# Optimization experiments

Measured on AMD Instinct MI355X. Metric: run time of the kernel, lower is better.

Reference implementation:

```python
import jax, jax.numpy as jnp
import numpy as np

B, S, D, KC = 32, 4096, 64, 256  # batch*heads, seq_len, head_dim, compressed dim


def setup_inputs() -> dict:
    key = jax.random.key(0)
    ks = jax.random.split(key, 7)
    return {
        "Q": jax.random.normal(ks[0], (B, S, D), dtype=jnp.float32),
        "K": jax.random.normal(ks[1], (B, S, D), dtype=jnp.float32),
        "V": jax.random.normal(ks[2], (B, S, D), dtype=jnp.float32),
        "E_w": jax.random.normal(ks[3], (KC, S), dtype=jnp.float32) * (1.0 / np.sqrt(S)),
        "E_b": jax.random.normal(ks[4], (KC,), dtype=jnp.float32) * 0.01,
        "F_w": jax.random.normal(ks[5], (KC, S), dtype=jnp.float32) * (1.0 / np.sqrt(S)),
        "F_b": jax.random.normal(ks[6], (KC,), dtype=jnp.float32) * 0.01,
    }


def reference(Q, K, V, E_w, E_b, F_w, F_b):
    # K: [B,S,D] -> transpose -> [B,D,S]; E proj over seq axis -> [B,D,KC]
    Ke = jnp.einsum("bsd,ks->bdk", K, E_w) + E_b  # [B, D, KC]
    # scores: Q @ E(K) -> [B, S, KC], scaled by sqrt(head_dim)
    scale = jnp.sqrt(jnp.asarray(D, dtype=Q.dtype))
    P = jnp.einsum("bsd,bdk->bsk", Q, Ke) / scale
    # causal mask: torch.triu(ones(S, KC)) keeps (i, j) where j >= i
    i = jnp.arange(S)[:, None]
    j = jnp.arange(KC)[None, :]
    keep = j >= i  # [S, KC]
    P = jnp.where(keep[None, :, :], P, jnp.asarray(-1e10, dtype=P.dtype))
    P = jax.nn.softmax(P, axis=-1)  # dropout p=0.0 -> identity
    # V: [B,S,D] -> [B,D,S]; F proj -> [B,D,KC]; transpose -> [B,KC,D]
    Vf = jnp.einsum("bsd,ks->bkd", V, F_w) + F_b[None, :, None]  # [B, KC, D]
    out = jnp.einsum("bsk,bkd->bsd", P, Vf)  # [B, S, D]
    return out
```

## Files before the change

kernel.cpp:

```cpp
#include <hip/hip_runtime.h>
#include <hip/hip_bf16.h>
#include <math.h>

#define NB  32
#define NS  4096
#define ND  64
#define NKC 256

#define BK   128
#define KHALF 2048
#define ASA  132
#define ASB  132

#define QSTR  72
#define PBSTR 264
#define VSTR  264

typedef __attribute__((ext_vector_type(8))) short short8;
typedef __attribute__((ext_vector_type(4))) float f32x4;

__device__ __forceinline__ short f2bf(float f) {
    union { float f; unsigned u; } v; v.f = f;
    return (short)((v.u + 0x7FFFu + ((v.u >> 16) & 1u)) >> 16);
}

__global__ __launch_bounds__(256) void prep(
    const float* __restrict__ Ew, const float* __restrict__ Fw,
    short* __restrict__ EwB, short* __restrict__ FwB)
{
    const int gid = blockIdx.x * 256 + threadIdx.x;
    const int half = (NKC * NS) / 8;
    const float* src = (gid < half) ? Ew : Fw;
    short* dst       = (gid < half) ? EwB : FwB;
    const int i8 = (gid < half) ? gid : gid - half;
    float4 a = *(const float4*)&src[(size_t)i8 * 8];
    float4 c = *(const float4*)&src[(size_t)i8 * 8 + 4];
    short8 w;
    w[0] = f2bf(a.x); w[1] = f2bf(a.y); w[2] = f2bf(a.z); w[3] = f2bf(a.w);
    w[4] = f2bf(c.x); w[5] = f2bf(c.y); w[6] = f2bf(c.z); w[7] = f2bf(c.w);
    *(short8*)&dst[(size_t)i8 * 8] = w;
}

template <typename AT>
__global__ __launch_bounds__(256, 2) void proj_sk(
    const AT* __restrict__ EwX, const AT* __restrict__ FwX,
    const float* __restrict__ K, const float* __restrict__ V,
    float* __restrict__ KeTa, float* __restrict__ Vfa,
    float* __restrict__ KeTb, float* __restrict__ Vfb)
{
    const int bid = blockIdx.x;
    const int r8 = bid & 7, mt = (bid >> 3) & 3, gq = bid >> 5;
    const int grp = gq * 8 + r8;
    const int kh = grp & 1, mm = (grp >> 1) & 1, b = grp >> 2;

    const AT* __restrict__ Ab    = mm ? FwX : EwX;
    const float* __restrict__ Bg = mm ? V   : K;
    float* __restrict__ Cout = kh ? (mm ? Vfb : KeTb) : (mm ? Vfa : KeTa);

    const int t = threadIdx.x, wave = t >> 6, lane = t & 63;
    const int lm = lane & 15, g4 = lane >> 4;
    __shared__ short As[64 * ASA];
    __shared__ short Bs[64 * ASB];
    const size_t bBase = (size_t)b * NS * ND;
    const size_t aBase = (size_t)mt * 64 * NS;
    const int rA = t >> 4, jA = t & 15;
    const int dB = t & 31, sB = t >> 5;

    f32x4 acc[4];
#pragma unroll
    for (int nt = 0; nt < 4; ++nt) acc[nt] = (f32x4){0.f, 0.f, 0.f, 0.f};

    short8 pa[4];
    float4 paf[8];
    float2 pb[16];

    const int sBeg = kh * KHALF, sEnd = sBeg + KHALF;

#pragma unroll
    for (int i = 0; i < 4; ++i) {
        if constexpr (sizeof(AT) == 2) {
            pa[i] = *(const short8*)&Ab[aBase + (size_t)(i * 16 + rA) * NS + sBeg + jA * 8];
        } else {
            paf[2 * i]     = *(const float4*)&Ab[aBase + (size_t)(i * 16 + rA) * NS + sBeg + jA * 8];
            paf[2 * i + 1] = *(const float4*)&Ab[aBase + (size_t)(i * 16 + rA) * NS + sBeg + jA * 8 + 4];
        }
    }
#pragma unroll
    for (int h = 0; h < 2; ++h)
#pragma unroll
        for (int i = 0; i < 8; ++i)
            pb[h * 8 + i] = *(const float2*)&Bg[bBase + (size_t)(sBeg + h * 64 + sB * 8 + i) * ND + dB * 2];

    for (int s0 = sBeg; s0 < sEnd; s0 += BK) {
#pragma unroll
        for (int i = 0; i < 4; ++i) {
            if constexpr (sizeof(AT) == 2) {
                *(short8*)&As[(i * 16 + rA) * ASA + jA * 8] = pa[i];
            } else {
                short8 w;
                w[0] = f2bf(paf[2 * i].x);     w[1] = f2bf(paf[2 * i].y);
                w[2] = f2bf(paf[2 * i].z);     w[3] = f2bf(paf[2 * i].w);
                w[4] = f2bf(paf[2 * i + 1].x); w[5] = f2bf(paf[2 * i + 1].y);
                w[6] = f2bf(paf[2 * i + 1].z); w[7] = f2bf(paf[2 * i + 1].w);
                *(short8*)&As[(i * 16 + rA) * ASA + jA * 8] = w;
            }
        }
#pragma unroll
        for (int h = 0; h < 2; ++h) {
            short8 w0, w1;
#pragma unroll
            for (int i = 0; i < 8; ++i) {
                w0[i] = f2bf(pb[h * 8 + i].x);
                w1[i] = f2bf(pb[h * 8 + i].y);
            }
            *(short8*)&Bs[(dB * 2 + 0) * ASB + h * 64 + sB * 8] = w0;
            *(short8*)&Bs[(dB * 2 + 1) * ASB + h * 64 + sB * 8] = w1;
        }
        __syncthreads();

        if (s0 + BK < sEnd) {
            const int sn = s0 + BK;
#pragma unroll
            for (int i = 0; i < 4; ++i) {
                if constexpr (sizeof(AT) == 2) {
                    pa[i] = *(const short8*)&Ab[aBase + (size_t)(i * 16 + rA) * NS + sn + jA * 8];
                } else {
                    paf[2 * i]     = *(const float4*)&Ab[aBase + (size_t)(i * 16 + rA) * NS + sn + jA * 8];
                    paf[2 * i + 1] = *(const float4*)&Ab[aBase + (size_t)(i * 16 + rA) * NS + sn + jA * 8 + 4];
                }
            }
#pragma unroll
            for (int h = 0; h < 2; ++h)
#pragma unroll
                for (int i = 0; i < 8; ++i)
                    pb[h * 8 + i] = *(const float2*)&Bg[bBase + (size_t)(sn + h * 64 + sB * 8 + i) * ND + dB * 2];
        }

#pragma unroll
        for (int ks = 0; ks < BK; ks += 32) {
            short8 aF = *(const short8*)&As[(wave * 16 + lm) * ASA + ks + g4 * 8];
#pragma unroll
            for (int nt = 0; nt < 4; ++nt) {
                short8 bF = *(const short8*)&Bs[(nt * 16 + lm) * ASB + ks + g4 * 8];
                acc[nt] = __builtin_amdgcn_mfma_f32_16x16x32_bf16(aF, bF, acc[nt], 0, 0, 0);
            }
        }
        __syncthreads();
    }

#pragma unroll
    for (int nt = 0; nt < 4; ++nt)
#pragma unroll
        for (int rr = 0; rr < 4; ++rr) {
            int kc = mt * 64 + wave * 16 + g4 * 4 + rr;
            Cout[((size_t)b * NKC + kc) * ND + nt * 16 + lm] = acc[nt][rr];
        }
}

__global__ __launch_bounds__(256) void reduce2(
    float4* __restrict__ Areg, const float4* __restrict__ Breg)
{
    const int gid = blockIdx.x * 256 + threadIdx.x;
    float4 a = Areg[gid], c = Breg[gid];
    Areg[gid] = (float4){a.x + c.x, a.y + c.y, a.z + c.z, a.w + c.w};
}

__global__ __launch_bounds__(256) void attn_fused(
    const float* __restrict__ Q,  const float* __restrict__ KeT,
    const float* __restrict__ Vf, const float* __restrict__ Eb,
    const float* __restrict__ Fb, float* __restrict__ out)
{
    const int x = blockIdx.x, b = blockIdx.y, t = threadIdx.x;

    if (x >= 8) {
        __shared__ float pq[16][64];
        __shared__ float mv[64];
        const int kg = t >> 4, dq = t & 15;
        float4 s4 = (float4){0.f, 0.f, 0.f, 0.f};
        for (int p = 0; p < 16; ++p) {
            int k = p * 16 + kg;
            float4 v = *(const float4*)&Vf[((size_t)b * NKC + k) * ND + dq * 4];
            float fb = Fb[k];
            s4.x += v.x + fb; s4.y += v.y + fb; s4.z += v.z + fb; s4.w += v.w + fb;
        }
        *(float4*)&pq[kg][dq * 4] = s4;
        __syncthreads();
        if (t < 64) {
            float m = 0.f;
#pragma unroll
            for (int i = 0; i < 16; ++i) m += pq[i][t];
            mv[t] = m * (1.f / 256.f);
        }
        __syncthreads();
        const int r0 = 256 + (x - 8) * 64;
#pragma unroll
        for (int i = 0; i < 4; ++i) {
            int idx = i * 256 + t, row = idx >> 4, q = idx & 15;
            *(float4*)&out[((size_t)b * NS + r0 + row) * ND + q * 4] =
                *(const float4*)&mv[q * 4];
        }
        return;
    }

    const int s0 = x * 32;
    const int wave = t >> 6, lane = t & 63, lm = lane & 15, g = lane >> 4;
    __shared__ short Qs[32 * QSTR];
    __shared__ short PsB[32 * PBSTR];
    __shared__ short VfT[64 * VSTR];
    __shared__ float rsums[32][4];

    {
        int row = t >> 3, dq = t & 7;
        size_t off = ((size_t)b * NS + s0 + row) * ND + dq * 8;
        float4 q0 = *(const float4*)&Q[off], q1 = *(const float4*)&Q[off + 4];
        short8 w;
        w[0] = f2bf(q0.x); w[1] = f2bf(q0.y); w[2] = f2bf(q0.z); w[3] = f2bf(q0.w);
        w[4] = f2bf(q1.x); w[5] = f2bf(q1.y); w[6] = f2bf(q1.z); w[7] = f2bf(q1.w);
        *(short8*)&Qs[row * QSTR + dq * 8] = w;
    }
    {
        const int dB = t & 31, sB = t >> 5;
#pragma unroll
        for (int pass = 0; pass < 4; ++pass) {
            int kb = pass * 64 + sB * 8;
            float2 v[8]; float fb[8];
#pragma unroll
            for (int i = 0; i < 8; ++i) {
                v[i]  = *(const float2*)&Vf[((size_t)b * NKC + kb + i) * ND + dB * 2];
                fb[i] = Fb[kb + i];
            }
            short8 w0, w1;
#pragma unroll
            for (int i = 0; i < 8; ++i) {
                w0[i] = f2bf(v[i].x + fb[i]);
                w1[i] = f2bf(v[i].y + fb[i]);
            }
            *(short8*)&VfT[(dB * 2 + 0) * VSTR + kb] = w0;
            *(short8*)&VfT[(dB * 2 + 1) * VSTR + kb] = w1;
        }
    }
    __syncthreads();

    f32x4 accP[2][4];
#pragma unroll
    for (int rt = 0; rt < 2; ++rt)
#pragma unroll
        for (int kk = 0; kk < 4; ++kk) accP[rt][kk] = (f32x4){0.f, 0.f, 0.f, 0.f};
#pragma unroll
    for (int kk = 0; kk < 4; ++kk) {
        int kt = wave * 4 + kk;
        float ebv = Eb[kt * 16 + lm];
#pragma unroll
        for (int ks2 = 0; ks2 < 2; ++ks2) {
            const float* kp = &KeT[((size_t)b * NKC + kt * 16 + lm) * ND + ks2 * 32 + g * 8];
            float4 c0 = *(const float4*)kp, c1 = *(const float4*)(kp + 4);
            short8 bf;
            bf[0] = f2bf(c0.x + ebv); bf[1] = f2bf(c0.y + ebv);
            bf[2] = f2bf(c0.z + ebv); bf[3] = f2bf(c0.w + ebv);
            bf[4] = f2bf(c1.x + ebv); bf[5] = f2bf(c1.y + ebv);
            bf[6] = f2bf(c1.z + ebv); bf[7] = f2bf(c1.w + ebv);
#pragma unroll
            for (int rt = 0; rt < 2; ++rt) {
                short8 aq = *(const short8*)&Qs[(rt * 16 + lm) * QSTR + ks2 * 32 + g * 8];
                accP[rt][kk] = __builtin_amdgcn_mfma_f32_16x16x32_bf16(aq, bf, accP[rt][kk], 0, 0, 0);
            }
        }
    }
#pragma unroll
    for (int rt = 0; rt < 2; ++rt)
#pragma unroll
        for (int r = 0; r < 4; ++r) {
            float s = 0.f;
            int rowg = s0 + rt * 16 + g * 4 + r;
#pragma unroll
            for (int kk = 0; kk < 4; ++kk) {
                int col = wave * 64 + kk * 16 + lm;
                float e = (col >= rowg) ? __expf(accP[rt][kk][r] * 0.125f) : 0.f;
                accP[rt][kk][r] = e;
                s += e;
            }
#pragma unroll
            for (int off = 1; off <= 8; off <<= 1) s += __shfl_xor(s, off, 64);
            if (lm == 0) rsums[rt * 16 + g * 4 + r][wave] = s;
        }
    __syncthreads();
#pragma unroll
    for (int rt = 0; rt < 2; ++rt)
#pragma unroll
        for (int r = 0; r < 4; ++r) {
            float4 rs = *(const float4*)&rsums[rt * 16 + g * 4 + r][0];
            float inv = 1.f / (rs.x + rs.y + rs.z + rs.w);
#pragma unroll
            for (int kk = 0; kk < 4; ++kk)
                PsB[(rt * 16 + g * 4 + r) * PBSTR + wave * 64 + kk * 16 + lm] =
                    f2bf(accP[rt][kk][r] * inv);
        }
    __syncthreads();

    f32x4 oa[2];
    oa[0] = (f32x4){0.f, 0.f, 0.f, 0.f};
    oa[1] = (f32x4){0.f, 0.f, 0.f, 0.f};
    for (int ks = x; ks < 8; ++ks) {
        short8 bv = *(const short8*)&VfT[(wave * 16 + lm) * VSTR + ks * 32 + g * 8];
#pragma unroll
        for (int rt = 0; rt < 2; ++rt) {
            short8 av = *(const short8*)&PsB[(rt * 16 + lm) * PBSTR + ks * 32 + g * 8];
            oa[rt] = __builtin_amdgcn_mfma_f32_16x16x32_bf16(av, bv, oa[rt], 0, 0, 0);
        }
    }
#pragma unroll
    for (int rt = 0; rt < 2; ++rt)
#pragma unroll
        for (int r = 0; r < 4; ++r)
            out[((size_t)b * NS + s0 + rt * 16 + g * 4 + r) * ND + wave * 16 + lm] = oa[rt][r];
}

extern "C" void kernel_launch(void* const* d_in, const int* in_sizes, int n_in,
                              void* d_out, int out_size, void* d_ws, size_t ws_size,
                              hipStream_t stream) {
    (void)in_sizes; (void)n_in; (void)out_size;
    const float* Q  = (const float*)d_in[0];
    const float* K  = (const float*)d_in[1];
    const float* V  = (const float*)d_in[2];
    const float* Ew = (const float*)d_in[3];
    const float* Eb = (const float*)d_in[4];
    const float* Fw = (const float*)d_in[5];
    const float* Fb = (const float*)d_in[6];
    float* out = (float*)d_out;

    const size_t nKe = (size_t)NB * NKC * ND;
    float* base = (float*)d_ws;
    float* KeTa = base;
    float* Vfa  = base + nKe;
    float* KeTb = base + 2 * nKe;
    float* Vfb  = base + 3 * nKe;

    if (ws_size >= 12u * 1024 * 1024) {
        short* EwB = (short*)(base + 4 * nKe);
        short* FwB = EwB + (size_t)NKC * NS;
        prep<<<dim3(1024), 256, 0, stream>>>(Ew, Fw, EwB, FwB);
        proj_sk<short><<<dim3(512), 256, 0, stream>>>(EwB, FwB, K, V,
                                                      KeTa, Vfa, KeTb, Vfb);
    } else {
        proj_sk<float><<<dim3(512), 256, 0, stream>>>(Ew, Fw, K, V,
                                                      KeTa, Vfa, KeTb, Vfb);
    }
    reduce2<<<dim3(1024), 256, 0, stream>>>((float4*)base,
                                            (const float4*)(base + 2 * nKe));
    attn_fused<<<dim3(68, NB), 256, 0, stream>>>(Q, KeTa, Vfa, Eb, Fb, out);
}
```

Measured before the change: 185.6 us.

## Drop weight prep, fuse split-K reduce with bias/bf16 conversion before attention

Removes the separate bf16 conversion pass over E_w/F_w, so proj_sk always reads fp32 weights directly. Replaces the reduce2 kernel with a fuse kernel that sums the two split-K halves, adds biases, and writes bf16 Ke and a pre-transposed bf16 Vf plus partial column sums. The attention kernel then loads ready bf16 tiles and reduces the partial sums for the masked-row mean instead of redoing conversion per block. This trades one conversion kernel for heavier fp32 weight traffic in the projection, and the workspace threshold decides which path runs.

```diff
diff --git a/kernel.cpp b/kernel.cpp
--- a/kernel.cpp
+++ b/kernel.cpp
@@ -7,46 +7,30 @@
 #define ND  64
 #define NKC 256
 
-#define BK   128
+#define BK    128
 #define KHALF 2048
-#define ASA  132
-#define ASB  132
+#define ASA   132
+#define ASB   132
 
 #define QSTR  72
 #define PBSTR 264
 #define VSTR  264
 
+#define NKE ((size_t)NB * NKC * ND)
+
 typedef __attribute__((ext_vector_type(8))) short short8;
 typedef __attribute__((ext_vector_type(4))) float f32x4;
 
 __device__ __forceinline__ short f2bf(float f) {
     union { float f; unsigned u; } v; v.f = f;
     return (short)((v.u + 0x7FFFu + ((v.u >> 16) & 1u)) >> 16);
-}
-
-__global__ __launch_bounds__(256) void prep(
-    const float* __restrict__ Ew, const float* __restrict__ Fw,
-    short* __restrict__ EwB, short* __restrict__ FwB)
-{
-    const int gid = blockIdx.x * 256 + threadIdx.x;
-    const int half = (NKC * NS) / 8;
-    const float* src = (gid < half) ? Ew : Fw;
-    short* dst       = (gid < half) ? EwB : FwB;
-    const int i8 = (gid < half) ? gid : gid - half;
-    float4 a = *(const float4*)&src[(size_t)i8 * 8];
-    float4 c = *(const float4*)&src[(size_t)i8 * 8 + 4];
-    short8 w;
-    w[0] = f2bf(a.x); w[1] = f2bf(a.y); w[2] = f2bf(a.z); w[3] = f2bf(a.w);
-    w[4] = f2bf(c.x); w[5] = f2bf(c.y); w[6] = f2bf(c.z); w[7] = f2bf(c.w);
-    *(short8*)&dst[(size_t)i8 * 8] = w;
 }
 
 template <typename AT>
 __global__ __launch_bounds__(256, 2) void proj_sk(
     const AT* __restrict__ EwX, const AT* __restrict__ FwX,
     const float* __restrict__ K, const float* __restrict__ V,
-    float* __restrict__ KeTa, float* __restrict__ Vfa,
-    float* __restrict__ KeTb, float* __restrict__ Vfb)
+    float* __restrict__ base)
 {
     const int bid = blockIdx.x;
     const int r8 = bid & 7, mt = (bid >> 3) & 3, gq = bid >> 5;
@@ -55,7 +39,7 @@
 
     const AT* __restrict__ Ab    = mm ? FwX : EwX;
     const float* __restrict__ Bg = mm ? V   : K;
-    float* __restrict__ Cout = kh ? (mm ? Vfb : KeTb) : (mm ? Vfa : KeTa);
+    float* __restrict__ Cout = base + (size_t)kh * 2 * NKE + (mm ? NKE : 0);
 
     const int t = threadIdx.x, wave = t >> 6, lane = t & 63;
     const int lm = lane & 15, g4 = lane >> 4;
@@ -157,39 +141,56 @@
         }
 }
 
-__global__ __launch_bounds__(256) void reduce2(
-    float4* __restrict__ Areg, const float4* __restrict__ Breg)
-{
-    const int gid = blockIdx.x * 256 + threadIdx.x;
-    float4 a = Areg[gid], c = Breg[gid];
-    Areg[gid] = (float4){a.x + c.x, a.y + c.y, a.z + c.z, a.w + c.w};
-}
-
-__global__ __launch_bounds__(256) void attn_fused(
-    const float* __restrict__ Q,  const float* __restrict__ KeT,
-    const float* __restrict__ Vf, const float* __restrict__ Eb,
-    const float* __restrict__ Fb, float* __restrict__ out)
+__global__ __launch_bounds__(256) void fuse(
+    const float* __restrict__ base, const float* __restrict__ Eb,
+    const float* __restrict__ Fb, short* __restrict__ KeB,
+    short* __restrict__ VtB, float* __restrict__ ps)
 {
     const int x = blockIdx.x, b = blockIdx.y, t = threadIdx.x;
+    const int kb = x * 16;
+    const float* Ka  = base;
+    const float* Va  = base + NKE;
+    const float* Kb_ = base + 2 * NKE;
+    const float* Vb  = base + 3 * NKE;
+    __shared__ float vt[16][65];
+    const int kci = t >> 6, d = t & 63;
+
+#pragma unroll
+    for (int i = 0; i < 4; ++i) {
+        int kc = kb + kci * 4 + i;
+        size_t off = ((size_t)b * NKC + kc) * ND + d;
+        KeB[off] = f2bf(Ka[off] + Kb_[off] + Eb[kc]);
+        vt[kci * 4 + i][d] = Va[off] + Vb[off] + Fb[kc];
+    }
+    __syncthreads();
+    if (t < 64) {
+        float s = 0.f;
+        short8 w0, w1;
+#pragma unroll
+        for (int i = 0; i < 8; ++i) { float v = vt[i][t];     s += v; w0[i] = f2bf(v); }
+#pragma unroll
+        for (int i = 0; i < 8; ++i) { float v = vt[8 + i][t]; s += v; w1[i] = f2bf(v); }
+        ps[((size_t)b * 16 + x) * 64 + t] = s;
+        short* dst = &VtB[((size_t)b * ND + t) * NKC + kb];
+        *(short8*)&dst[0] = w0;
+        *(short8*)&dst[8] = w1;
+    }
+}
+
+__global__ __launch_bounds__(256) void attn_new(
+    const float* __restrict__ Q,  const short* __restrict__ KeB,
+    const short* __restrict__ VtB, const float* __restrict__ ps,
+    float* __restrict__ out)
+{
+    const int x = blockIdx.x, b = blockIdx.y, t = threadIdx.x;
 
     if (x >= 8) {
-        __shared__ float pq[16][64];
-        __shared__ float mv[64];
-        const int kg = t >> 4, dq = t & 15;
-        float4 s4 = (float4){0.f, 0.f, 0.f, 0.f};
-        for (int p = 0; p < 16; ++p) {
-            int k = p * 16 + kg;
-            float4 v = *(const float4*)&Vf[((size_t)b * NKC + k) * ND + dq * 4];
-            float fb = Fb[k];
-            s4.x += v.x + fb; s4.y += v.y + fb; s4.z += v.z + fb; s4.w += v.w + fb;
-        }
-        *(float4*)&pq[kg][dq * 4] = s4;
-        __syncthreads();
+        __shared__ float mvs[64];
         if (t < 64) {
-            float m = 0.f;
-#pragma unroll
-            for (int i = 0; i < 16; ++i) m += pq[i][t];
-            mv[t] = m * (1.f / 256.f);
+            float s = 0.f;
+#pragma unroll
+            for (int i = 0; i < 16; ++i) s += ps[((size_t)b * 16 + i) * 64 + t];
+            mvs[t] = s * (1.f / 256.f);
         }
         __syncthreads();
         const int r0 = 256 + (x - 8) * 64;
@@ -197,7 +198,7 @@
         for (int i = 0; i < 4; ++i) {
             int idx = i * 256 + t, row = idx >> 4, q = idx & 15;
             *(float4*)&out[((size_t)b * NS + r0 + row) * ND + q * 4] =
-                *(const float4*)&mv[q * 4];
+                *(const float4*)&mvs[q * 4];
         }
         return;
     }
@@ -219,6 +220,141 @@
         *(short8*)&Qs[row * QSTR + dq * 8] = w;
     }
     {
+        const int d = t >> 2, q4 = t & 3;
+        const short* src = &VtB[((size_t)b * ND + d) * NKC + q4 * 64];
+#pragma unroll
+        for (int i = 0; i < 8; ++i)
+            *(short8*)&VfT[d * VSTR + q4 * 64 + i * 8] = *(const short8*)&src[i * 8];
+    }
+    __syncthreads();
+
+    f32x4 accP[2][4];
+#pragma unroll
+    for (int rt = 0; rt < 2; ++rt)
+#pragma unroll
+        for (int kk = 0; kk < 4; ++kk) accP[rt][kk] = (f32x4){0.f, 0.f, 0.f, 0.f};
+#pragma unroll
+    for (int kk = 0; kk < 4; ++kk) {
+        int kt = wave * 4 + kk;
+#pragma unroll
+        for (int ks2 = 0; ks2 < 2; ++ks2) {
+            short8 bf = *(const short8*)&KeB[((size_t)b * NKC + kt * 16 + lm) * ND + ks2 * 32 + g * 8];
+#pragma unroll
+            for (int rt = 0; rt < 2; ++rt) {
+                short8 aq = *(const short8*)&Qs[(rt * 16 + lm) * QSTR + ks2 * 32 + g * 8];
+                accP[rt][kk] = __builtin_amdgcn_mfma_f32_16x16x32_bf16(aq, bf, accP[rt][kk], 0, 0, 0);
+            }
+        }
+    }
+#pragma unroll
+    for (int rt = 0; rt < 2; ++rt)
+#pragma unroll
+        for (int r = 0; r < 4; ++r) {
+            float s = 0.f;
+            int rowg = s0 + rt * 16 + g * 4 + r;
+#pragma unroll
+            for (int kk = 0; kk < 4; ++kk) {
+                int col = wave * 64 + kk * 16 + lm;
+                float e = (col >= rowg) ? __expf(accP[rt][kk][r] * 0.125f) : 0.f;
+                accP[rt][kk][r] = e;
+                s += e;
+            }
+#pragma unroll
+            for (int off = 1; off <= 8; off <<= 1) s += __shfl_xor(s, off, 64);
+            if (lm == 0) rsums[rt * 16 + g * 4 + r][wave] = s;
+        }
+    __syncthreads();
+#pragma unroll
+    for (int rt = 0; rt < 2; ++rt)
+#pragma unroll
+        for (int r = 0; r < 4; ++r) {
+            float4 rs = *(const float4*)&rsums[rt * 16 + g * 4 + r][0];
+            float inv = 1.f / (rs.x + rs.y + rs.z + rs.w);
+#pragma unroll
+            for (int kk = 0; kk < 4; ++kk)
+                PsB[(rt * 16 + g * 4 + r) * PBSTR + wave * 64 + kk * 16 + lm] =
+                    f2bf(accP[rt][kk][r] * inv);
+        }
+    __syncthreads();
+
+    f32x4 oa[2];
+    oa[0] = (f32x4){0.f, 0.f, 0.f, 0.f};
+    oa[1] = (f32x4){0.f, 0.f, 0.f, 0.f};
+    for (int ks = x; ks < 8; ++ks) {
+        short8 bv = *(const short8*)&VfT[(wave * 16 + lm) * VSTR + ks * 32 + g * 8];
+#pragma unroll
+        for (int rt = 0; rt < 2; ++rt) {
+            short8 av = *(const short8*)&PsB[(rt * 16 + lm) * PBSTR + ks * 32 + g * 8];
+            oa[rt] = __builtin_amdgcn_mfma_f32_16x16x32_bf16(av, bv, oa[rt], 0, 0, 0);
+        }
+    }
+#pragma unroll
+    for (int rt = 0; rt < 2; ++rt)
+#pragma unroll
+        for (int r = 0; r < 4; ++r)
+            out[((size_t)b * NS + s0 + rt * 16 + g * 4 + r) * ND + wave * 16 + lm] = oa[rt][r];
+}
+
+__global__ __launch_bounds__(256) void attn_old(
+    const float* __restrict__ Q,  const float* __restrict__ base,
+    const float* __restrict__ Eb, const float* __restrict__ Fb,
+    float* __restrict__ out)
+{
+    const int x = blockIdx.x, b = blockIdx.y, t = threadIdx.x;
+    const float* KeTa = base;
+    const float* Vfa  = base + NKE;
+    const float* KeTb = base + 2 * NKE;
+    const float* Vfb  = base + 3 * NKE;
+
+    if (x >= 8) {
+        __shared__ float pq[16][64];
+        __shared__ float mvs[64];
+        const int kg = t >> 4, dq = t & 15;
+        float4 s4 = (float4){0.f, 0.f, 0.f, 0.f};
+        for (int p = 0; p < 16; ++p) {
+            int k = p * 16 + kg;
+            float4 v = *(const float4*)&Vfa[((size_t)b * NKC + k) * ND + dq * 4];
+            float4 u = *(const float4*)&Vfb[((size_t)b * NKC + k) * ND + dq * 4];
+            float fb = Fb[k];
+            s4.x += (v.x + u.x) + fb; s4.y += (v.y + u.y) + fb;
+            s4.z += (v.z + u.z) + fb; s4.w += (v.w + u.w) + fb;
+        }
+        *(float4*)&pq[kg][dq * 4] = s4;
+        __syncthreads();
+        if (t < 64) {
+            float m = 0.f;
+#pragma unroll
+            for (int i = 0; i < 16; ++i) m += pq[i][t];
+            mvs[t] = m * (1.f / 256.f);
+        }
+        __syncthreads();
+        const int r0 = 256 + (x - 8) * 64;
+#pragma unroll
+        for (int i = 0; i < 4; ++i) {
+            int idx = i * 256 + t, row = idx >> 4, q = idx & 15;
+            *(float4*)&out[((size_t)b * NS + r0 + row) * ND + q * 4] =
+                *(const float4*)&mvs[q * 4];
+        }
+        return;
+    }
+
+    const int s0 = x * 32;
+    const int wave = t >> 6, lane = t & 63, lm = lane & 15, g = lane >> 4;
+    __shared__ short Qs[32 * QSTR];
+    __shared__ short PsB[32 * PBSTR];
+    __shared__ short VfT[64 * VSTR];
+    __shared__ float rsums[32][4];
+
+    {
+        int row = t >> 3, dq = t & 7;
+        size_t off = ((size_t)b * NS + s0 + row) * ND + dq * 8;
+        float4 q0 = *(const float4*)&Q[off], q1 = *(const float4*)&Q[off + 4];
+        short8 w;
+        w[0] = f2bf(q0.x); w[1] = f2bf(q0.y); w[2] = f2bf(q0.z); w[3] = f2bf(q0.w);
+        w[4] = f2bf(q1.x); w[5] = f2bf(q1.y); w[6] = f2bf(q1.z); w[7] = f2bf(q1.w);
+        *(short8*)&Qs[row * QSTR + dq * 8] = w;
+    }
+    {
         const int dB = t & 31, sB = t >> 5;
 #pragma unroll
         for (int pass = 0; pass < 4; ++pass) {
@@ -226,7 +362,9 @@
             float2 v[8]; float fb[8];
 #pragma unroll
             for (int i = 0; i < 8; ++i) {
-                v[i]  = *(const float2*)&Vf[((size_t)b * NKC + kb + i) * ND + dB * 2];
+                float2 a = *(const float2*)&Vfa[((size_t)b * NKC + kb + i) * ND + dB * 2];
+                float2 c = *(const float2*)&Vfb[((size_t)b * NKC + kb + i) * ND + dB * 2];
+                v[i]  = (float2){a.x + c.x, a.y + c.y};
                 fb[i] = Fb[kb + i];
             }
             short8 w0, w1;
@@ -252,13 +390,14 @@
         float ebv = Eb[kt * 16 + lm];
 #pragma unroll
         for (int ks2 = 0; ks2 < 2; ++ks2) {
-            const float* kp = &KeT[((size_t)b * NKC + kt * 16 + lm) * ND + ks2 * 32 + g * 8];
-            float4 c0 = *(const float4*)kp, c1 = *(const float4*)(kp + 4);
+            const size_t koff = ((size_t)b * NKC + kt * 16 + lm) * ND + ks2 * 32 + g * 8;
+            float4 c0 = *(const float4*)&KeTa[koff], c1 = *(const float4*)&KeTa[koff + 4];
+            float4 e0 = *(const float4*)&KeTb[koff], e1 = *(const float4*)&KeTb[koff + 4];
             short8 bf;
-            bf[0] = f2bf(c0.x + ebv); bf[1] = f2bf(c0.y + ebv);
-            bf[2] = f2bf(c0.z + ebv); bf[3] = f2bf(c0.w + ebv);
-            bf[4] = f2bf(c1.x + ebv); bf[5] = f2bf(c1.y + ebv);
-            bf[6] = f2bf(c1.z + ebv); bf[7] = f2bf(c1.w + ebv);
+            bf[0] = f2bf((c0.x + e0.x) + ebv); bf[1] = f2bf((c0.y + e0.y) + ebv);
+            bf[2] = f2bf((c0.z + e0.z) + ebv); bf[3] = f2bf((c0.w + e0.w) + ebv);
+            bf[4] = f2bf((c1.x + e1.x) + ebv); bf[5] = f2bf((c1.y + e1.y) + ebv);
+            bf[6] = f2bf((c1.z + e1.z) + ebv); bf[7] = f2bf((c1.w + e1.w) + ebv);
 #pragma unroll
             for (int rt = 0; rt < 2; ++rt) {
                 short8 aq = *(const short8*)&Qs[(rt * 16 + lm) * QSTR + ks2 * 32 + g * 8];
@@ -328,24 +467,18 @@
     const float* Fb = (const float*)d_in[6];
     float* out = (float*)d_out;
 
-    const size_t nKe = (size_t)NB * NKC * ND;
     float* base = (float*)d_ws;
-    float* KeTa = base;
-    float* Vfa  = base + nKe;
-    float* KeTb = base + 2 * nKe;
-    float* Vfb  = base + 3 * nKe;
-
-    if (ws_size >= 12u * 1024 * 1024) {
-        short* EwB = (short*)(base + 4 * nKe);
-        short* FwB = EwB + (size_t)NKC * NS;
-        prep<<<dim3(1024), 256, 0, stream>>>(Ew, Fw, EwB, FwB);
-        proj_sk<short><<<dim3(512), 256, 0, stream>>>(EwB, FwB, K, V,
-                                                      KeTa, Vfa, KeTb, Vfb);
+    const size_t MB = 1024u * 1024u;
+
+    proj_sk<float><<<dim3(512), 256, 0, stream>>>(Ew, Fw, K, V, base);
+
+    if (ws_size >= 11 * MB) {
+        short* KeB = (short*)(base + 4 * NKE);
+        short* VtB = KeB + NKE;
+        float* ps  = (float*)(VtB + NKE);
+        fuse<<<dim3(16, NB), 256, 0, stream>>>(base, Eb, Fb, KeB, VtB, ps);
+        attn_new<<<dim3(68, NB), 256, 0, stream>>>(Q, KeB, VtB, ps, out);
     } else {
-        proj_sk<float><<<dim3(512), 256, 0, stream>>>(Ew, Fw, K, V,
-                                                      KeTa, Vfa, KeTb, Vfb);
-    }
-    reduce2<<<dim3(1024), 256, 0, stream>>>((float4*)base,
-                                            (const float4*)(base + 2 * nKe));
-    attn_fused<<<dim3(68, NB), 256, 0, stream>>>(Q, KeTa, Vfa, Eb, Fb, out);
-}
+        attn_old<<<dim3(68, NB), 256, 0, stream>>>(Q, base, Eb, Fb, out);
+    }
+}
```

After: 183.7 us. About the same (-1.1%).
